# Kernel optimization log

Measured on AMD Instinct MI355X. Metric: run time of the kernel, lower is better.

## Reference

```python
import jax, jax.numpy as jnp
import numpy as np

N, DEG, FIN, HID, OUT = 50000, 16, 128, 128, 64


def setup_inputs() -> dict:
    key = jax.random.key(0)
    ks = jax.random.split(key, 32)
    x = jax.random.normal(ks[0], (N, FIN), dtype=jnp.float32)
    src = jax.random.randint(ks[1], (N * DEG,), 0, N, dtype=jnp.int32)
    dst = jnp.repeat(jnp.arange(N, dtype=jnp.int32), DEG)  # sorted by target, fixed degree
    edge_index = jnp.stack([src, dst])  # [2, E]
    dims = [(FIN, HID), (HID, HID), (HID, OUT)]
    params = {}
    i = 2
    for l, (fi, fo) in enumerate(dims, 1):
        s_lstm = 1.0 / np.sqrt(fi)
        params[f"W_ih{l}"] = jax.random.normal(ks[i + 0], (4 * fi, fi)) * s_lstm
        params[f"W_hh{l}"] = jax.random.normal(ks[i + 1], (4 * fi, fi)) * s_lstm
        params[f"b_ih{l}"] = jax.random.normal(ks[i + 2], (4 * fi,)) * s_lstm
        params[f"b_hh{l}"] = jax.random.normal(ks[i + 3], (4 * fi,)) * s_lstm
        params[f"Wl{l}"] = jax.random.normal(ks[i + 4], (fo, fi)) * (1.0 / np.sqrt(fi))
        params[f"bl{l}"] = jnp.zeros((fo,), jnp.float32)
        params[f"Wr{l}"] = jax.random.normal(ks[i + 5], (fo, fi)) * (1.0 / np.sqrt(fi))
        i += 6
    return {"x": x, "edge_index": edge_index, **params}


def _lstm_last(neigh, Wih, Whh, bih, bhh):
    # neigh: [N, deg, Fi]; PyTorch LSTM gate order i,f,g,o; return last-step output h.
    h0 = jnp.zeros((neigh.shape[0], Wih.shape[0] // 4), neigh.dtype)
    bias = bih + bhh

    def step(carry, xt):
        h, c = carry
        g = xt @ Wih.T + h @ Whh.T + bias
        i, f, gg, o = jnp.split(g, 4, axis=-1)
        c = jax.nn.sigmoid(f) * c + jax.nn.sigmoid(i) * jnp.tanh(gg)
        h = jax.nn.sigmoid(o) * jnp.tanh(c)
        return (h, c), None

    (h, _), _ = jax.lax.scan(step, (h0, h0), jnp.swapaxes(neigh, 0, 1))
    return h


def _sage_layer(x, src2d, Wih, Whh, bih, bhh, Wl, bl, Wr):
    neigh = x[src2d]  # gather: [N, deg, Fi]
    aggr = _lstm_last(neigh, Wih, Whh, bih, bhh)  # [N, Fi]
    return aggr @ Wl.T + bl + x @ Wr.T  # lin_l(aggr) + lin_r(x)


def reference(x, edge_index,
              W_ih1, W_hh1, b_ih1, b_hh1, Wl1, bl1, Wr1,
              W_ih2, W_hh2, b_ih2, b_hh2, Wl2, bl2, Wr2,
              W_ih3, W_hh3, b_ih3, b_hh3, Wl3, bl3, Wr3):
    n = x.shape[0]
    src2d = edge_index[0].reshape(n, -1)  # fixed-degree, dst-sorted edge list
    h = _sage_layer(x, src2d, W_ih1, W_hh1, b_ih1, b_hh1, Wl1, bl1, Wr1)
    h = jax.nn.relu(h)  # dropout is identity in eval mode
    h = _sage_layer(h, src2d, W_ih2, W_hh2, b_ih2, b_hh2, Wl2, bl2, Wr2)
    h = jax.nn.relu(h)
    return _sage_layer(h, src2d, W_ih3, W_hh3, b_ih3, b_hh3, Wl3, bl3, Wr3)
```

## Files before the change

### kernel.cpp

```cpp
#include <hip/hip_runtime.h>
#include <cstddef>
#include <cstdint>

typedef __attribute__((ext_vector_type(4))) float f32x4;
typedef __attribute__((ext_vector_type(8))) short short8;

#define HID 128
#define NK1 -1.4426950408889634f
#define PK2 2.8853900817779268f

#define BAR_LGKM() __asm__ volatile("s_waitcnt lgkmcnt(0)\ns_barrier" ::: "memory")
#define STEP_BAR2() __asm__ volatile("s_waitcnt vmcnt(2) lgkmcnt(0)\ns_barrier" ::: "memory")

__device__ __forceinline__ short f2bf(float f) {
  unsigned u = __builtin_bit_cast(unsigned, f);
  u += 0x7FFFu + ((u >> 16) & 1u);
  return (short)(u >> 16);
}
__device__ __forceinline__ unsigned pack_bf2(float a, float b) {
  unsigned ua = __builtin_bit_cast(unsigned, a) + 0x8000u;
  unsigned ub = __builtin_bit_cast(unsigned, b) + 0x8000u;
  return __builtin_amdgcn_perm(ub, ua, 0x07060302u);
}
__device__ __forceinline__ float2 unpack2v(int w) {
  float2 r;
  r.x = __builtin_bit_cast(float, (unsigned)(w << 16));
  r.y = __builtin_bit_cast(float, (unsigned)w & 0xffff0000u);
  return r;
}

__device__ __forceinline__ float lstm_elem(float si, float sf, float sg, float so, float& c) {
  float Ei = __builtin_amdgcn_exp2f(si);
  float Ef = __builtin_amdgcn_exp2f(sf);
  float Tg = __builtin_amdgcn_exp2f(sg);
  float Eo = __builtin_amdgcn_exp2f(so);
  float u = 1.0f + Ei, w = 1.0f + Ef, v = Tg + 1.0f, Tm = Tg - 1.0f;
  float t0 = u * v;
  float num = __builtin_fmaf(c, t0, w * Tm);
  float cn = num * __builtin_amdgcn_rcpf(w * t0);
  c = cn;
  float Tc = __builtin_amdgcn_exp2f(PK2 * cn);
  return (Tc - 1.0f) * __builtin_amdgcn_rcpf((1.0f + Eo) * (Tc + 1.0f));
}

__global__ void conv_x_kernel(const float* __restrict__ x, short* __restrict__ xb, int n) {
  int i = blockIdx.x * blockDim.x + threadIdx.x;
  int stride = gridDim.x * blockDim.x;
  for (; i < n; i += stride) xb[i] = f2bf(x[i]);
}

__global__ void conv_layer_kernel(const float* __restrict__ Wih, const float* __restrict__ Whh,
                                  const float* __restrict__ bih, const float* __restrict__ bhh,
                                  const float* __restrict__ Wl, const float* __restrict__ Wr, int foK,
                                  short* __restrict__ wihB, short* __restrict__ whhB,
                                  short* __restrict__ wlB, short* __restrict__ wrB,
                                  float* __restrict__ bsum) {
  int i = blockIdx.x * blockDim.x + threadIdx.x;
  if (i < 512 * HID) {
    float sc = ((i >> 14) == 2) ? PK2 : NK1;
    wihB[i] = f2bf(Wih[i] * sc);
    whhB[i] = f2bf(Whh[i] * sc);
  }
  if (i < foK) { wlB[i] = f2bf(Wl[i]); wrB[i] = f2bf(Wr[i]); }
  if (i < 512) bsum[i] = (bih[i] + bhh[i]) * (((i >> 7) == 2) ? PK2 : NK1);
}

#define OSTR 524
__global__ __launch_bounds__(512, 4) void pgemm_kernel(
    const short* __restrict__ A, const short* __restrict__ W,
    const float* __restrict__ bias, short* __restrict__ out, int M, int ntiles) {
  __shared__ short ldsO[32 * OSTR];
  const int tid = threadIdx.x;
  const int wave = tid >> 6, lane = tid & 63;
  const int quad = lane >> 4, nn = lane & 15;
  const int cbase = wave * 64;

  short8 wreg[4][4];
#pragma unroll
  for (int kt = 0; kt < 4; ++kt)
#pragma unroll
    for (int nt = 0; nt < 4; ++nt)
      wreg[kt][nt] = *(const short8*)(W + (size_t)(cbase + nt * 16 + nn) * HID + kt * 32 + quad * 8);
  f32x4 bias4[4];
#pragma unroll
  for (int nt = 0; nt < 4; ++nt)
#pragma unroll
    for (int r = 0; r < 4; ++r) bias4[nt][r] = bias[cbase + nt * 16 + quad * 4 + r];

#pragma unroll 1
  for (int rt = blockIdx.x; rt < ntiles; rt += gridDim.x) {
    const int row0 = rt * 32;
    f32x4 acc[2][4];
#pragma unroll
    for (int b = 0; b < 2; ++b)
#pragma unroll
      for (int nt = 0; nt < 4; ++nt) acc[b][nt] = bias4[nt];
#pragma unroll
    for (int kt = 0; kt < 4; ++kt) {
      int r0 = row0 + nn;      if (r0 > M - 1) r0 = M - 1;
      int r1 = row0 + 16 + nn; if (r1 > M - 1) r1 = M - 1;
      short8 af0 = *(const short8*)(A + (size_t)r0 * HID + kt * 32 + quad * 8);
      short8 af1 = *(const short8*)(A + (size_t)r1 * HID + kt * 32 + quad * 8);
#pragma unroll
      for (int nt = 0; nt < 4; ++nt) {
        acc[0][nt] = __builtin_amdgcn_mfma_f32_16x16x32_bf16(wreg[kt][nt], af0, acc[0][nt], 0, 0, 0);
        acc[1][nt] = __builtin_amdgcn_mfma_f32_16x16x32_bf16(wreg[kt][nt], af1, acc[1][nt], 0, 0, 0);
      }
    }
    BAR_LGKM();
#pragma unroll
    for (int b = 0; b < 2; ++b)
#pragma unroll
      for (int nt = 0; nt < 4; ++nt) {
        uint2 pk;
        pk.x = pack_bf2(acc[b][nt][0], acc[b][nt][1]);
        pk.y = pack_bf2(acc[b][nt][2], acc[b][nt][3]);
        *(uint2*)(ldsO + (b * 16 + nn) * OSTR + cbase + nt * 16 + quad * 4) = pk;
      }
    BAR_LGKM();
#pragma unroll
    for (int idx = tid; idx < 32 * 64; idx += 512) {
      int row = idx >> 6, c8 = (idx & 63) * 8;
      if (row0 + row < M)
        *(short8*)(out + (size_t)(row0 + row) * 512 + c8) = *(const short8*)(ldsO + row * OSTR + c8);
    }
  }
}

#define NPB 16
#define PSTR 520
#define HSTR 152
#define LSTM_LDS_BYTES ((3 * NPB * PSTR + 2 * NPB * HSTR) * 2 + 256 * 4)

template <int FO, bool RELU, bool OUTF32>
__global__ __launch_bounds__(512, 4) void lstm_fused_kernel(
    const short* __restrict__ P, const short* __restrict__ Whh,
    const int* __restrict__ src, const short* __restrict__ cur,
    const short* __restrict__ Wl, const short* __restrict__ Wr,
    const float* __restrict__ bl,
    short* __restrict__ outB, float* __restrict__ outF, int M, int ntiles) {
  extern __shared__ char smem[];
  short* Pb = (short*)smem;
  short* Hb = Pb + 3 * NPB * PSTR;
  int* srcL = (int*)(Hb + 2 * NPB * HSTR);

  const int tid = threadIdx.x;
  const int wave = tid >> 6, lane = tid & 63;
  const int quad = lane >> 4, nn = lane & 15;
  const int r0row = wave * 2, r1row = wave * 2 + 1;

  short8 wreg[4][4];
#pragma unroll
  for (int kt = 0; kt < 4; ++kt)
#pragma unroll
    for (int q = 0; q < 4; ++q)
      wreg[kt][q] = *(const short8*)(Whh + (size_t)(q * 128 + wave * 16 + nn) * HID + kt * 32 + quad * 8);

  f32x4 biasO = {0.f, 0.f, 0.f, 0.f};
  if (FO == 128 || wave < 4) {
#pragma unroll
    for (int r = 0; r < 4; ++r) biasO[r] = bl[wave * 16 + quad * 4 + r];
  }

#pragma unroll 1
  for (int tile = blockIdx.x; tile < ntiles; tile += gridDim.x) {
    const int nodeBase = tile * NPB;
    if (tid < 256) {
      int node = nodeBase + (tid >> 4);
      srcL[tid] = (node < M) ? src[nodeBase * 16 + tid] : 0;
    }
    float c_st[4] = {0.f, 0.f, 0.f, 0.f};
    BAR_LGKM();

    {
      int s0A = srcL[r0row * 16 + 0], s0B = srcL[r1row * 16 + 0];
      __builtin_amdgcn_global_load_lds(
          (const __attribute__((address_space(1))) unsigned int*)(P + (size_t)s0A * 512 + lane * 8),
          (__attribute__((address_space(3))) unsigned int*)(Pb + r0row * PSTR), 16, 0, 0);
      __builtin_amdgcn_global_load_lds(
          (const __attribute__((address_space(1))) unsigned int*)(P + (size_t)s0B * 512 + lane * 8),
          (__attribute__((address_space(3))) unsigned int*)(Pb + r1row * PSTR), 16, 0, 0);
      int s1A = srcL[r0row * 16 + 1], s1B = srcL[r1row * 16 + 1];
      __builtin_amdgcn_global_load_lds(
          (const __attribute__((address_space(1))) unsigned int*)(P + (size_t)s1A * 512 + lane * 8),
          (__attribute__((address_space(3))) unsigned int*)(Pb + NPB * PSTR + r0row * PSTR), 16, 0, 0);
      __builtin_amdgcn_global_load_lds(
          (const __attribute__((address_space(1))) unsigned int*)(P + (size_t)s1B * 512 + lane * 8),
          (__attribute__((address_space(3))) unsigned int*)(Pb + NPB * PSTR + r1row * PSTR), 16, 0, 0);
    }
    int sA = srcL[r0row * 16 + 2], sB = srcL[r1row * 16 + 2];

    int pc = 0, pg = 2;
#pragma unroll 1
    for (int t = 0; t < 16; ++t) {
      short* Pc = Pb + pc * NPB * PSTR;
      short* Pg = Pb + pg * NPB * PSTR;
      const short* Hp = Hb + ((t + 1) & 1) * NPB * HSTR;
      short* Hw = Hb + (t & 1) * NPB * HSTR;
      pc = (pc == 2) ? 0 : pc + 1;
      pg = (pg == 2) ? 0 : pg + 1;

      STEP_BAR2();

      const short* pR = Pc + nn * PSTR + wave * 16 + quad * 4;
      uint2 p0 = *(const uint2*)(pR + 0 * 128);
      uint2 p1 = *(const uint2*)(pR + 1 * 128);
      uint2 p2 = *(const uint2*)(pR + 2 * 128);
      uint2 p3 = *(const uint2*)(pR + 3 * 128);
      f32x4 acc[4];
      {
        float2 u, v;
        u = unpack2v(p0.x); v = unpack2v(p0.y);
        acc[0][0] = u.x; acc[0][1] = u.y; acc[0][2] = v.x; acc[0][3] = v.y;
        u = unpack2v(p1.x); v = unpack2v(p1.y);
        acc[1][0] = u.x; acc[1][1] = u.y; acc[1][2] = v.x; acc[1][3] = v.y;
        u = unpack2v(p2.x); v = unpack2v(p2.y);
        acc[2][0] = u.x; acc[2][1] = u.y; acc[2][2] = v.x; acc[2][3] = v.y;
        u = unpack2v(p3.x); v = unpack2v(p3.y);
        acc[3][0] = u.x; acc[3][1] = u.y; acc[3][2] = v.x; acc[3][3] = v.y;
      }

      __builtin_amdgcn_global_load_lds(
          (const __attribute__((address_space(1))) unsigned int*)(P + (size_t)sA * 512 + lane * 8),
          (__attribute__((address_space(3))) unsigned int*)(Pg + r0row * PSTR), 16, 0, 0);
      __builtin_amdgcn_global_load_lds(
          (const __attribute__((address_space(1))) unsigned int*)(P + (size_t)sB * 512 + lane * 8),
          (__attribute__((address_space(3))) unsigned int*)(Pg + r1row * PSTR), 16, 0, 0);
      {
        int tn = (t + 3 < 16) ? t + 3 : 15;
        sA = srcL[r0row * 16 + tn];
        sB = srcL[r1row * 16 + tn];
      }

      if (t) {
#pragma unroll
        for (int kt = 0; kt < 4; ++kt) {
          short8 hb = *(const short8*)(Hp + nn * HSTR + kt * 32 + quad * 8);
#pragma unroll
          for (int q = 0; q < 4; ++q)
            acc[q] = __builtin_amdgcn_mfma_f32_16x16x32_bf16(wreg[kt][q], hb, acc[q], 0, 0, 0);
        }
      }

      float hv[4];
#pragma unroll
      for (int r = 0; r < 4; ++r)
        hv[r] = lstm_elem(acc[0][r], acc[1][r], acc[2][r], acc[3][r], c_st[r]);
      uint2 pk;
      pk.x = pack_bf2(hv[0], hv[1]);
      pk.y = pack_bf2(hv[2], hv[3]);
      *(uint2*)(Hw + nn * HSTR + wave * 16 + quad * 4) = pk;
    }

    BAR_LGKM();

    if (FO == 128 || wave < 4) {
      const short* Hf = Hb + NPB * HSTR;
      const int cbase = wave * 16;
      f32x4 accO = biasO;
#pragma unroll
      for (int kt = 0; kt < 4; ++kt) {
        short8 wlA = *(const short8*)(Wl + (size_t)(cbase + nn) * HID + kt * 32 + quad * 8);
        short8 hb = *(const short8*)(Hf + nn * HSTR + kt * 32 + quad * 8);
        accO = __builtin_amdgcn_mfma_f32_16x16x32_bf16(wlA, hb, accO, 0, 0, 0);
        short8 wrA = *(const short8*)(Wr + (size_t)(cbase + nn) * HID + kt * 32 + quad * 8);
        short8 cb = *(const short8*)(cur + (size_t)(nodeBase + nn) * HID + kt * 32 + quad * 8);
        accO = __builtin_amdgcn_mfma_f32_16x16x32_bf16(wrA, cb, accO, 0, 0, 0);
      }
      if (RELU) {
#pragma unroll
        for (int r = 0; r < 4; ++r) accO[r] = fmaxf(accO[r], 0.0f);
      }
      int node = nodeBase + nn;
      if (node < M) {
        if (OUTF32) {
          *(f32x4*)(outF + (size_t)node * FO + cbase + quad * 4) = accO;
        } else {
          uint2 pko;
          pko.x = pack_bf2(accO[0], accO[1]);
          pko.y = pack_bf2(accO[2], accO[3]);
          *(uint2*)(outB + (size_t)node * FO + cbase + quad * 4) = pko;
        }
      }
    }
  }
}

extern "C" void kernel_launch(void* const* d_in, const int* in_sizes, int n_in,
                              void* d_out, int out_size, void* d_ws, size_t ws_size,
                              hipStream_t stream) {
  const float* x = (const float*)d_in[0];
  const int* src = (const int*)d_in[1];
  const float* Wih[3] = {(const float*)d_in[2], (const float*)d_in[9], (const float*)d_in[16]};
  const float* Whh[3] = {(const float*)d_in[3], (const float*)d_in[10], (const float*)d_in[17]};
  const float* bih[3] = {(const float*)d_in[4], (const float*)d_in[11], (const float*)d_in[18]};
  const float* bhh[3] = {(const float*)d_in[5], (const float*)d_in[12], (const float*)d_in[19]};
  const float* Wl[3]  = {(const float*)d_in[6], (const float*)d_in[13], (const float*)d_in[20]};
  const float* bl[3]  = {(const float*)d_in[7], (const float*)d_in[14], (const float*)d_in[21]};
  const float* Wr[3]  = {(const float*)d_in[8], (const float*)d_in[15], (const float*)d_in[22]};

  const int M = in_sizes[0] / HID;

  char* ws = (char*)d_ws;
  size_t off = 0;
  auto alloc = [&](size_t bytes) -> void* {
    void* p = ws + off;
    off += (bytes + 255) & ~(size_t)255;
    return p;
  };
  short* curA = (short*)alloc((size_t)M * HID * 2);
  short* curB = (short*)alloc((size_t)M * HID * 2);
  short* Pbuf = (short*)alloc((size_t)M * 512 * 2);
  short* wihB[3]; short* whhB[3]; short* wlB[3]; short* wrB[3]; float* bsum[3];
  for (int l = 0; l < 3; ++l) {
    wihB[l] = (short*)alloc(512 * HID * 2);
    whhB[l] = (short*)alloc(512 * HID * 2);
    wlB[l]  = (short*)alloc(HID * HID * 2);
    wrB[l]  = (short*)alloc(HID * HID * 2);
    bsum[l] = (float*)alloc(512 * 4);
  }

  const int nltiles = (M + NPB - 1) / NPB;
  const int ntiles = (M + 31) / 32;

  (void)hipFuncSetAttribute((const void*)lstm_fused_kernel<128, true, false>,
                            hipFuncAttributeMaxDynamicSharedMemorySize, LSTM_LDS_BYTES);
  (void)hipFuncSetAttribute((const void*)lstm_fused_kernel<64, false, true>,
                            hipFuncAttributeMaxDynamicSharedMemorySize, LSTM_LDS_BYTES);

  conv_x_kernel<<<2048, 256, 0, stream>>>(x, curA, M * HID);
  for (int l = 0; l < 3; ++l) {
    const int Fo = (l == 2) ? 64 : 128;
    conv_layer_kernel<<<256, 256, 0, stream>>>(Wih[l], Whh[l], bih[l], bhh[l], Wl[l], Wr[l],
                                               Fo * HID, wihB[l], whhB[l], wlB[l], wrB[l], bsum[l]);
  }

  short* cur = curA;
  short* nxt = curB;
  for (int l = 0; l < 3; ++l) {
    pgemm_kernel<<<784, 512, 0, stream>>>(cur, wihB[l], bsum[l], Pbuf, M, ntiles);
    if (l < 2) {
      lstm_fused_kernel<128, true, false><<<512, 512, LSTM_LDS_BYTES, stream>>>(
          Pbuf, whhB[l], src, cur, wlB[l], wrB[l], bl[l], nxt, nullptr, M, nltiles);
      short* tswap = cur; cur = nxt; nxt = tswap;
    } else {
      lstm_fused_kernel<64, false, true><<<512, 512, LSTM_LDS_BYTES, stream>>>(
          Pbuf, whhB[l], src, cur, wlB[l], wrB[l], bl[l], nullptr, (float*)d_out, M, nltiles);
    }
  }
}
```

Before: 759.0 us.

## Load gathered gate rows directly to registers and schedule LSTM tiles dynamically

The triple-buffered LDS staging of gathered P rows (global_load_lds plus a vmcnt barrier per step) is replaced by direct per-lane register loads of each lane's own gate slice, prefetched one step ahead. The src index layout in LDS is transposed to suit the new access. Tiles are now handed out by an atomic work counter, reset in conv_x_kernel, instead of a static grid-stride loop, and LDS drops to a small static allocation. The aim is less LDS traffic and better occupancy and load balance, at the cost of only one step of prefetch to hide gather latency.

```diff
diff --git a/kernel.cpp b/kernel.cpp
--- a/kernel.cpp
+++ b/kernel.cpp
@@ -10,7 +10,6 @@
 #define PK2 2.8853900817779268f
 
 #define BAR_LGKM() __asm__ volatile("s_waitcnt lgkmcnt(0)\ns_barrier" ::: "memory")
-#define STEP_BAR2() __asm__ volatile("s_waitcnt vmcnt(2) lgkmcnt(0)\ns_barrier" ::: "memory")
 
 __device__ __forceinline__ short f2bf(float f) {
   unsigned u = __builtin_bit_cast(unsigned, f);
@@ -43,8 +42,10 @@
   return (Tc - 1.0f) * __builtin_amdgcn_rcpf((1.0f + Eo) * (Tc + 1.0f));
 }
 
-__global__ void conv_x_kernel(const float* __restrict__ x, short* __restrict__ xb, int n) {
+__global__ void conv_x_kernel(const float* __restrict__ x, short* __restrict__ xb, int n,
+                              int* __restrict__ tctr) {
   int i = blockIdx.x * blockDim.x + threadIdx.x;
+  if (i < 8) tctr[i] = 0;
   int stride = gridDim.x * blockDim.x;
   for (; i < n; i += stride) xb[i] = f2bf(x[i]);
 }
@@ -128,9 +129,7 @@
 }
 
 #define NPB 16
-#define PSTR 520
 #define HSTR 152
-#define LSTM_LDS_BYTES ((3 * NPB * PSTR + 2 * NPB * HSTR) * 2 + 256 * 4)
 
 template <int FO, bool RELU, bool OUTF32>
 __global__ __launch_bounds__(512, 4) void lstm_fused_kernel(
@@ -138,16 +137,15 @@
     const int* __restrict__ src, const short* __restrict__ cur,
     const short* __restrict__ Wl, const short* __restrict__ Wr,
     const float* __restrict__ bl,
-    short* __restrict__ outB, float* __restrict__ outF, int M, int ntiles) {
-  extern __shared__ char smem[];
-  short* Pb = (short*)smem;
-  short* Hb = Pb + 3 * NPB * PSTR;
-  int* srcL = (int*)(Hb + 2 * NPB * HSTR);
+    short* __restrict__ outB, float* __restrict__ outF, int M, int ntiles,
+    int* __restrict__ tctr) {
+  __shared__ short Hb[2 * NPB * HSTR];
+  __shared__ int srcL[256];
+  __shared__ int nextT;
 
   const int tid = threadIdx.x;
   const int wave = tid >> 6, lane = tid & 63;
   const int quad = lane >> 4, nn = lane & 15;
-  const int r0row = wave * 2, r1row = wave * 2 + 1;
 
   short8 wreg[4][4];
 #pragma unroll
@@ -162,51 +160,35 @@
     for (int r = 0; r < 4; ++r) biasO[r] = bl[wave * 16 + quad * 4 + r];
   }
 
-#pragma unroll 1
-  for (int tile = blockIdx.x; tile < ntiles; tile += gridDim.x) {
+  const short* Pl = P + wave * 16 + quad * 4;
+
+  int tile = blockIdx.x;
+  while (tile < ntiles) {
     const int nodeBase = tile * NPB;
     if (tid < 256) {
-      int node = nodeBase + (tid >> 4);
-      srcL[tid] = (node < M) ? src[nodeBase * 16 + tid] : 0;
-    }
+      int node = nodeBase + (tid & 15);
+      srcL[tid] = (node < M) ? src[nodeBase * 16 + ((tid & 15) << 4) + (tid >> 4)] : 0;
+    }
+    if (tid == 0) nextT = (int)gridDim.x + atomicAdd(tctr, 1);
     float c_st[4] = {0.f, 0.f, 0.f, 0.f};
     BAR_LGKM();
-
+    const int my_next = nextT;
+
+    uint2 p0, p1, p2, p3;
     {
-      int s0A = srcL[r0row * 16 + 0], s0B = srcL[r1row * 16 + 0];
-      __builtin_amdgcn_global_load_lds(
-          (const __attribute__((address_space(1))) unsigned int*)(P + (size_t)s0A * 512 + lane * 8),
-          (__attribute__((address_space(3))) unsigned int*)(Pb + r0row * PSTR), 16, 0, 0);
-      __builtin_amdgcn_global_load_lds(
-          (const __attribute__((address_space(1))) unsigned int*)(P + (size_t)s0B * 512 + lane * 8),
-          (__attribute__((address_space(3))) unsigned int*)(Pb + r1row * PSTR), 16, 0, 0);
-      int s1A = srcL[r0row * 16 + 1], s1B = srcL[r1row * 16 + 1];
-      __builtin_amdgcn_global_load_lds(
-          (const __attribute__((address_space(1))) unsigned int*)(P + (size_t)s1A * 512 + lane * 8),
-          (__attribute__((address_space(3))) unsigned int*)(Pb + NPB * PSTR + r0row * PSTR), 16, 0, 0);
-      __builtin_amdgcn_global_load_lds(
-          (const __attribute__((address_space(1))) unsigned int*)(P + (size_t)s1B * 512 + lane * 8),
-          (__attribute__((address_space(3))) unsigned int*)(Pb + NPB * PSTR + r1row * PSTR), 16, 0, 0);
-    }
-    int sA = srcL[r0row * 16 + 2], sB = srcL[r1row * 16 + 2];
-
-    int pc = 0, pg = 2;
+      int s = srcL[nn];
+      const short* pb = Pl + (size_t)s * 512;
+      p0 = *(const uint2*)(pb);
+      p1 = *(const uint2*)(pb + 128);
+      p2 = *(const uint2*)(pb + 256);
+      p3 = *(const uint2*)(pb + 384);
+    }
+
 #pragma unroll 1
     for (int t = 0; t < 16; ++t) {
-      short* Pc = Pb + pc * NPB * PSTR;
-      short* Pg = Pb + pg * NPB * PSTR;
       const short* Hp = Hb + ((t + 1) & 1) * NPB * HSTR;
       short* Hw = Hb + (t & 1) * NPB * HSTR;
-      pc = (pc == 2) ? 0 : pc + 1;
-      pg = (pg == 2) ? 0 : pg + 1;
-
-      STEP_BAR2();
-
-      const short* pR = Pc + nn * PSTR + wave * 16 + quad * 4;
-      uint2 p0 = *(const uint2*)(pR + 0 * 128);
-      uint2 p1 = *(const uint2*)(pR + 1 * 128);
-      uint2 p2 = *(const uint2*)(pR + 2 * 128);
-      uint2 p3 = *(const uint2*)(pR + 3 * 128);
+
       f32x4 acc[4];
       {
         float2 u, v;
@@ -220,16 +202,13 @@
         acc[3][0] = u.x; acc[3][1] = u.y; acc[3][2] = v.x; acc[3][3] = v.y;
       }
 
-      __builtin_amdgcn_global_load_lds(
-          (const __attribute__((address_space(1))) unsigned int*)(P + (size_t)sA * 512 + lane * 8),
-          (__attribute__((address_space(3))) unsigned int*)(Pg + r0row * PSTR), 16, 0, 0);
-      __builtin_amdgcn_global_load_lds(
-          (const __attribute__((address_space(1))) unsigned int*)(P + (size_t)sB * 512 + lane * 8),
-          (__attribute__((address_space(3))) unsigned int*)(Pg + r1row * PSTR), 16, 0, 0);
-      {
-        int tn = (t + 3 < 16) ? t + 3 : 15;
-        sA = srcL[r0row * 16 + tn];
-        sB = srcL[r1row * 16 + tn];
+      if (t < 15) {
+        int s = srcL[(t + 1) * 16 + nn];
+        const short* pb = Pl + (size_t)s * 512;
+        p0 = *(const uint2*)(pb);
+        p1 = *(const uint2*)(pb + 128);
+        p2 = *(const uint2*)(pb + 256);
+        p3 = *(const uint2*)(pb + 384);
       }
 
       if (t) {
@@ -250,9 +229,8 @@
       pk.x = pack_bf2(hv[0], hv[1]);
       pk.y = pack_bf2(hv[2], hv[3]);
       *(uint2*)(Hw + nn * HSTR + wave * 16 + quad * 4) = pk;
-    }
-
-    BAR_LGKM();
+      BAR_LGKM();
+    }
 
     if (FO == 128 || wave < 4) {
       const short* Hf = Hb + NPB * HSTR;
@@ -283,6 +261,7 @@
         }
       }
     }
+    tile = my_next;
   }
 }
 
@@ -319,16 +298,12 @@
     wrB[l]  = (short*)alloc(HID * HID * 2);
     bsum[l] = (float*)alloc(512 * 4);
   }
+  int* tctr = (int*)alloc(256);
 
   const int nltiles = (M + NPB - 1) / NPB;
   const int ntiles = (M + 31) / 32;
 
-  (void)hipFuncSetAttribute((const void*)lstm_fused_kernel<128, true, false>,
-                            hipFuncAttributeMaxDynamicSharedMemorySize, LSTM_LDS_BYTES);
-  (void)hipFuncSetAttribute((const void*)lstm_fused_kernel<64, false, true>,
-                            hipFuncAttributeMaxDynamicSharedMemorySize, LSTM_LDS_BYTES);
-
-  conv_x_kernel<<<2048, 256, 0, stream>>>(x, curA, M * HID);
+  conv_x_kernel<<<2048, 256, 0, stream>>>(x, curA, M * HID, tctr);
   for (int l = 0; l < 3; ++l) {
     const int Fo = (l == 2) ? 64 : 128;
     conv_layer_kernel<<<256, 256, 0, stream>>>(Wih[l], Whh[l], bih[l], bhh[l], Wl[l], Wr[l],
@@ -340,12 +315,12 @@
   for (int l = 0; l < 3; ++l) {
     pgemm_kernel<<<784, 512, 0, stream>>>(cur, wihB[l], bsum[l], Pbuf, M, ntiles);
     if (l < 2) {
-      lstm_fused_kernel<128, true, false><<<512, 512, LSTM_LDS_BYTES, stream>>>(
-          Pbuf, whhB[l], src, cur, wlB[l], wrB[l], bl[l], nxt, nullptr, M, nltiles);
+      lstm_fused_kernel<128, true, false><<<512, 512, 0, stream>>>(
+          Pbuf, whhB[l], src, cur, wlB[l], wrB[l], bl[l], nxt, nullptr, M, nltiles, tctr + l);
       short* tswap = cur; cur = nxt; nxt = tswap;
     } else {
-      lstm_fused_kernel<64, false, true><<<512, 512, LSTM_LDS_BYTES, stream>>>(
-          Pbuf, whhB[l], src, cur, wlB[l], wrB[l], bl[l], nullptr, (float*)d_out, M, nltiles);
-    }
-  }
-}
+      lstm_fused_kernel<64, false, true><<<512, 512, 0, stream>>>(
+          Pbuf, whhB[l], src, cur, wlB[l], wrB[l], bl[l], nullptr, (float*)d_out, M, nltiles, tctr + 2);
+    }
+  }
+}
```

Result: slower. 929.6 us (+22.5%).

## Deepen LSTM gather prefetch to 4 stages, add dynamic tile scheduling, cache Wl/Wr

Applied to the files above, without the earlier changes.

The fused LSTM kernel grows its LDS ring buffer for gathered gate pre-activations from 3 to 4 slots, prefetching 3 timesteps ahead and waiting with vmcnt(4). A global atomic counter, zeroed in the conversion kernel, now hands out tiles dynamically instead of a static grid stride, to balance work across blocks. The Wl/Wr output-projection weights are loaded once into registers instead of being reloaded per tile. The extra LDS slot and register use may lower occupancy, and the atomic adds a small serialization point per tile.

```diff
diff --git a/kernel.cpp b/kernel.cpp
--- a/kernel.cpp
+++ b/kernel.cpp
@@ -10,7 +10,7 @@
 #define PK2 2.8853900817779268f
 
 #define BAR_LGKM() __asm__ volatile("s_waitcnt lgkmcnt(0)\ns_barrier" ::: "memory")
-#define STEP_BAR2() __asm__ volatile("s_waitcnt vmcnt(2) lgkmcnt(0)\ns_barrier" ::: "memory")
+#define STEP_BAR3() __asm__ volatile("s_waitcnt vmcnt(4) lgkmcnt(0)\ns_barrier" ::: "memory")
 
 __device__ __forceinline__ short f2bf(float f) {
   unsigned u = __builtin_bit_cast(unsigned, f);
@@ -43,8 +43,10 @@
   return (Tc - 1.0f) * __builtin_amdgcn_rcpf((1.0f + Eo) * (Tc + 1.0f));
 }
 
-__global__ void conv_x_kernel(const float* __restrict__ x, short* __restrict__ xb, int n) {
+__global__ void conv_x_kernel(const float* __restrict__ x, short* __restrict__ xb, int n,
+                              int* __restrict__ tctr) {
   int i = blockIdx.x * blockDim.x + threadIdx.x;
+  if (i < 8) tctr[i] = 0;
   int stride = gridDim.x * blockDim.x;
   for (; i < n; i += stride) xb[i] = f2bf(x[i]);
 }
@@ -130,7 +132,7 @@
 #define NPB 16
 #define PSTR 520
 #define HSTR 152
-#define LSTM_LDS_BYTES ((3 * NPB * PSTR + 2 * NPB * HSTR) * 2 + 256 * 4)
+#define LSTM_LDS_BYTES ((4 * NPB * PSTR + 2 * NPB * HSTR) * 2 + 256 * 4 + 16)
 
 template <int FO, bool RELU, bool OUTF32>
 __global__ __launch_bounds__(512, 4) void lstm_fused_kernel(
@@ -138,11 +140,13 @@
     const int* __restrict__ src, const short* __restrict__ cur,
     const short* __restrict__ Wl, const short* __restrict__ Wr,
     const float* __restrict__ bl,
-    short* __restrict__ outB, float* __restrict__ outF, int M, int ntiles) {
+    short* __restrict__ outB, float* __restrict__ outF, int M, int ntiles,
+    int* __restrict__ tctr) {
   extern __shared__ char smem[];
   short* Pb = (short*)smem;
-  short* Hb = Pb + 3 * NPB * PSTR;
+  short* Hb = Pb + 4 * NPB * PSTR;
   int* srcL = (int*)(Hb + 2 * NPB * HSTR);
+  int* nextTp = srcL + 256;
 
   const int tid = threadIdx.x;
   const int wave = tid >> 6, lane = tid & 63;
@@ -157,50 +161,52 @@
       wreg[kt][q] = *(const short8*)(Whh + (size_t)(q * 128 + wave * 16 + nn) * HID + kt * 32 + quad * 8);
 
   f32x4 biasO = {0.f, 0.f, 0.f, 0.f};
+  short8 wlR[4], wrR[4];
   if (FO == 128 || wave < 4) {
 #pragma unroll
     for (int r = 0; r < 4; ++r) biasO[r] = bl[wave * 16 + quad * 4 + r];
-  }
-
-#pragma unroll 1
-  for (int tile = blockIdx.x; tile < ntiles; tile += gridDim.x) {
+#pragma unroll
+    for (int kt = 0; kt < 4; ++kt) {
+      wlR[kt] = *(const short8*)(Wl + (size_t)(wave * 16 + nn) * HID + kt * 32 + quad * 8);
+      wrR[kt] = *(const short8*)(Wr + (size_t)(wave * 16 + nn) * HID + kt * 32 + quad * 8);
+    }
+  }
+
+  int tile = blockIdx.x;
+  while (tile < ntiles) {
     const int nodeBase = tile * NPB;
     if (tid < 256) {
       int node = nodeBase + (tid >> 4);
       srcL[tid] = (node < M) ? src[nodeBase * 16 + tid] : 0;
     }
+    if (tid == 0) *nextTp = (int)gridDim.x + atomicAdd(tctr, 1);
     float c_st[4] = {0.f, 0.f, 0.f, 0.f};
     BAR_LGKM();
-
-    {
-      int s0A = srcL[r0row * 16 + 0], s0B = srcL[r1row * 16 + 0];
+    const int my_next = *nextTp;
+
+#pragma unroll
+    for (int tt = 0; tt < 3; ++tt) {
+      int sa = srcL[r0row * 16 + tt], sb = srcL[r1row * 16 + tt];
       __builtin_amdgcn_global_load_lds(
-          (const __attribute__((address_space(1))) unsigned int*)(P + (size_t)s0A * 512 + lane * 8),
-          (__attribute__((address_space(3))) unsigned int*)(Pb + r0row * PSTR), 16, 0, 0);
+          (const __attribute__((address_space(1))) unsigned int*)(P + (size_t)sa * 512 + lane * 8),
+          (__attribute__((address_space(3))) unsigned int*)(Pb + tt * NPB * PSTR + r0row * PSTR), 16, 0, 0);
       __builtin_amdgcn_global_load_lds(
-          (const __attribute__((address_space(1))) unsigned int*)(P + (size_t)s0B * 512 + lane * 8),
-          (__attribute__((address_space(3))) unsigned int*)(Pb + r1row * PSTR), 16, 0, 0);
-      int s1A = srcL[r0row * 16 + 1], s1B = srcL[r1row * 16 + 1];
-      __builtin_amdgcn_global_load_lds(
-          (const __attribute__((address_space(1))) unsigned int*)(P + (size_t)s1A * 512 + lane * 8),
-          (__attribute__((address_space(3))) unsigned int*)(Pb + NPB * PSTR + r0row * PSTR), 16, 0, 0);
-      __builtin_amdgcn_global_load_lds(
-          (const __attribute__((address_space(1))) unsigned int*)(P + (size_t)s1B * 512 + lane * 8),
-          (__attribute__((address_space(3))) unsigned int*)(Pb + NPB * PSTR + r1row * PSTR), 16, 0, 0);
-    }
-    int sA = srcL[r0row * 16 + 2], sB = srcL[r1row * 16 + 2];
-
-    int pc = 0, pg = 2;
+          (const __attribute__((address_space(1))) unsigned int*)(P + (size_t)sb * 512 + lane * 8),
+          (__attribute__((address_space(3))) unsigned int*)(Pb + tt * NPB * PSTR + r1row * PSTR), 16, 0, 0);
+    }
+    int sA = srcL[r0row * 16 + 3], sB = srcL[r1row * 16 + 3];
+
+    int pc = 0, pg = 3;
 #pragma unroll 1
     for (int t = 0; t < 16; ++t) {
       short* Pc = Pb + pc * NPB * PSTR;
       short* Pg = Pb + pg * NPB * PSTR;
       const short* Hp = Hb + ((t + 1) & 1) * NPB * HSTR;
       short* Hw = Hb + (t & 1) * NPB * HSTR;
-      pc = (pc == 2) ? 0 : pc + 1;
-      pg = (pg == 2) ? 0 : pg + 1;
-
-      STEP_BAR2();
+      pc = (pc + 1) & 3;
+      pg = (pg + 1) & 3;
+
+      STEP_BAR3();
 
       const short* pR = Pc + nn * PSTR + wave * 16 + quad * 4;
       uint2 p0 = *(const uint2*)(pR + 0 * 128);
@@ -227,7 +233,7 @@
           (const __attribute__((address_space(1))) unsigned int*)(P + (size_t)sB * 512 + lane * 8),
           (__attribute__((address_space(3))) unsigned int*)(Pg + r1row * PSTR), 16, 0, 0);
       {
-        int tn = (t + 3 < 16) ? t + 3 : 15;
+        int tn = (t + 4 < 16) ? t + 4 : 15;
         sA = srcL[r0row * 16 + tn];
         sB = srcL[r1row * 16 + tn];
       }
@@ -260,12 +266,10 @@
       f32x4 accO = biasO;
 #pragma unroll
       for (int kt = 0; kt < 4; ++kt) {
-        short8 wlA = *(const short8*)(Wl + (size_t)(cbase + nn) * HID + kt * 32 + quad * 8);
         short8 hb = *(const short8*)(Hf + nn * HSTR + kt * 32 + quad * 8);
-        accO = __builtin_amdgcn_mfma_f32_16x16x32_bf16(wlA, hb, accO, 0, 0, 0);
-        short8 wrA = *(const short8*)(Wr + (size_t)(cbase + nn) * HID + kt * 32 + quad * 8);
+        accO = __builtin_amdgcn_mfma_f32_16x16x32_bf16(wlR[kt], hb, accO, 0, 0, 0);
         short8 cb = *(const short8*)(cur + (size_t)(nodeBase + nn) * HID + kt * 32 + quad * 8);
-        accO = __builtin_amdgcn_mfma_f32_16x16x32_bf16(wrA, cb, accO, 0, 0, 0);
+        accO = __builtin_amdgcn_mfma_f32_16x16x32_bf16(wrR[kt], cb, accO, 0, 0, 0);
       }
       if (RELU) {
 #pragma unroll
@@ -283,6 +287,7 @@
         }
       }
     }
+    tile = my_next;
   }
 }
 
@@ -319,6 +324,7 @@
     wrB[l]  = (short*)alloc(HID * HID * 2);
     bsum[l] = (float*)alloc(512 * 4);
   }
+  int* tctr = (int*)alloc(256);
 
   const int nltiles = (M + NPB - 1) / NPB;
   const int ntiles = (M + 31) / 32;
@@ -328,7 +334,7 @@
   (void)hipFuncSetAttribute((const void*)lstm_fused_kernel<64, false, true>,
                             hipFuncAttributeMaxDynamicSharedMemorySize, LSTM_LDS_BYTES);
 
-  conv_x_kernel<<<2048, 256, 0, stream>>>(x, curA, M * HID);
+  conv_x_kernel<<<2048, 256, 0, stream>>>(x, curA, M * HID, tctr);
   for (int l = 0; l < 3; ++l) {
     const int Fo = (l == 2) ? 64 : 128;
     conv_layer_kernel<<<256, 256, 0, stream>>>(Wih[l], Whh[l], bih[l], bhh[l], Wl[l], Wr[l],
@@ -341,11 +347,11 @@
     pgemm_kernel<<<784, 512, 0, stream>>>(cur, wihB[l], bsum[l], Pbuf, M, ntiles);
     if (l < 2) {
       lstm_fused_kernel<128, true, false><<<512, 512, LSTM_LDS_BYTES, stream>>>(
-          Pbuf, whhB[l], src, cur, wlB[l], wrB[l], bl[l], nxt, nullptr, M, nltiles);
+          Pbuf, whhB[l], src, cur, wlB[l], wrB[l], bl[l], nxt, nullptr, M, nltiles, tctr + l);
       short* tswap = cur; cur = nxt; nxt = tswap;
     } else {
       lstm_fused_kernel<64, false, true><<<512, 512, LSTM_LDS_BYTES, stream>>>(
-          Pbuf, whhB[l], src, cur, wlB[l], wrB[l], bl[l], nullptr, (float*)d_out, M, nltiles);
-    }
-  }
-}
+          Pbuf, whhB[l], src, cur, wlB[l], wrB[l], bl[l], nullptr, (float*)d_out, M, nltiles, tctr + 2);
+    }
+  }
+}
```

Measured after the change: 787.2 us. 1.04x slower.
